# Optimization experiments

Hardware: AMD Instinct MI355X
Metric: run time of the kernel (lower is better)

Reference implementation:

```python
import jax, jax.numpy as jnp
import numpy as np
from jax import lax

DIM = 256
NH = 16          # num_heads; head_dim = DIM//NH == NH (required by scale broadcast)
HD = DIM // NH   # 16
HID = int(DIM * 1.0)  # mlp hidden (ffn_expansion_factor=1.0)
B, H, W = 4, 128, 128
EPS = 1e-5


def _conv(x, w, pad, groups=1):
    # x: NCHW, w: OIHW
    return lax.conv_general_dilated(x, w, (1, 1), [(pad, pad), (pad, pad)],
                                    dimension_numbers=('NCHW', 'OIHW', 'NCHW'),
                                    feature_group_count=groups)


def _ln(x, w, b):
    # WithBias LayerNorm over channel axis (torch does it in b,(hw),c layout -> axis=c)
    mu = x.mean(1, keepdims=True)
    var = ((x - mu) ** 2).mean(1, keepdims=True)
    return (x - mu) / jnp.sqrt(var + EPS) * w[None, :, None, None] + b[None, :, None, None]


def setup_inputs() -> dict:
    key = jax.random.key(0)
    ks = jax.random.split(key, 12)
    s = 0.02
    return {
        'x': jax.random.normal(ks[0], (B, DIM, H, W), jnp.float32),
        'ln1_w': jnp.ones((DIM,), jnp.float32),
        'ln1_b': jnp.zeros((DIM,), jnp.float32),
        'conv3_w': jax.random.normal(ks[1], (DIM, 1, 3, 3), jnp.float32) * s,
        'conv3_b': jnp.zeros((DIM,), jnp.float32),
        'conv5_w': jax.random.normal(ks[2], (DIM, 1, 5, 5), jnp.float32) * s,
        'conv5_b': jnp.zeros((DIM,), jnp.float32),
        'qkv_w': jax.random.normal(ks[3], (3 * DIM, DIM), jnp.float32) * s,  # 1x1 conv, no bias
        'scale': jnp.ones((NH, 1, 1), jnp.float32),
        'g1_w': jax.random.normal(ks[4], (DIM // 4, DIM), jnp.float32) * s,
        'g1_b': jnp.zeros((DIM // 4,), jnp.float32),
        'g2_w': jax.random.normal(ks[5], (2, DIM // 4), jnp.float32) * s,
        'g2_b': jnp.zeros((2,), jnp.float32),
        'proj_w': jax.random.normal(ks[6], (DIM, DIM), jnp.float32) * s,
        'proj_b': jnp.zeros((DIM,), jnp.float32),
        'ln2_w': jnp.ones((DIM,), jnp.float32),
        'ln2_b': jnp.zeros((DIM,), jnp.float32),
        'pin_w': jax.random.normal(ks[7], (2 * HID, DIM), jnp.float32) * s,  # 1x1, bias=False
        'dw_w': jax.random.normal(ks[8], (2 * HID, 2, 3, 3), jnp.float32) * s,  # groups=HID
        'pout_w': jax.random.normal(ks[9], (DIM, HID), jnp.float32) * s,
    }


def _forward(x, ln1_w, ln1_b, conv3_w, conv3_b, conv5_w, conv5_b, qkv_w, scale,
             g1_w, g1_b, g2_w, g2_b, proj_w, proj_b, ln2_w, ln2_b, pin_w, dw_w, pout_w):
    b, c, h, w = x.shape
    # ---- token mixer (CAFormer) ----
    y = _ln(x, ln1_w, ln1_b)
    conv_feat = (_conv(y, conv3_w, 1, groups=DIM) + conv3_b[None, :, None, None]
                 + _conv(y, conv5_w, 2, groups=DIM) + conv5_b[None, :, None, None])
    qkv = jnp.einsum('oc,bchw->bohw', qkv_w, y)  # (b, 3c, h, w)
    q, k, v = jnp.split(qkv.reshape(b, 3, NH, HD, h * w), 3, axis=1)
    q, k, v = q[:, 0], k[:, 0], v[:, 0]  # (b, nh, hd, h*w)
    # L2 normalize over entire flattened spatial extent (F.normalize, eps=1e-12)
    q = q / jnp.maximum(jnp.linalg.norm(q, axis=-1, keepdims=True), 1e-12)
    k = k / jnp.maximum(jnp.linalg.norm(k, axis=-1, keepdims=True), 1e-12)
    q4 = q.reshape(b, NH, HD, h, w)
    k4 = k.reshape(b, NH, HD, h, w)
    v4 = v.reshape(b, NH, HD, h, w)
    # scale (nh,1,1) right-aligned against (b,nh,hd,x,x): broadcasts along hd axis
    sc = scale.reshape(1, 1, NH, 1, 1)
    # horizontal (row) attention: per (b,head,hd-channel), rows attend to rows
    attn_h = jax.nn.softmax(jnp.einsum('bhdxy,bhdzy->bhdxz', q4, k4) * sc, axis=-1)
    out_h = jnp.einsum('bhdxz,bhdzy->bhdxy', attn_h, v4).reshape(b, c, h, w)
    # vertical (column) attention
    qt, kt, vt = (t.swapaxes(-1, -2) for t in (q4, k4, v4))  # (b,nh,hd,w,h)
    attn_v = jax.nn.softmax(jnp.einsum('bhdyx,bhdzx->bhdyz', qt, kt) * sc, axis=-1)
    out_v = jnp.einsum('bhdyz,bhdzx->bhdyx', attn_v, vt).swapaxes(-1, -2).reshape(b, c, h, w)
    attn_feat = out_h + out_v
    # gate: GAP -> 1x1 -> relu -> 1x1 -> softmax over the 2 branch logits
    gp = y.mean((2, 3))  # (b, c)
    g = jax.nn.relu(gp @ g1_w.T + g1_b)
    g = jax.nn.softmax(g @ g2_w.T + g2_b, axis=-1)  # (b, 2)
    cw = g[:, 0][:, None, None, None]
    aw = g[:, 1][:, None, None, None]
    mixed = cw * conv_feat + aw * attn_feat
    tm = jnp.einsum('oc,bchw->bohw', proj_w, mixed) + proj_b[None, :, None, None]
    x = x + tm
    # ---- MLP ----
    y2 = _ln(x, ln2_w, ln2_b)
    p = jnp.einsum('oc,bchw->bohw', pin_w, y2)  # (b, 2*HID, h, w)
    dwo = _conv(p, dw_w, 1, groups=HID)         # grouped 3x3, 2 ch per group
    x1, x2 = dwo[:, :HID], dwo[:, HID:]
    m = jax.nn.gelu(x1, approximate=False) * x2
    mlp = jnp.einsum('oc,bchw->bohw', pout_w, m)
    return x + mlp


def reference(x, ln1_w, ln1_b, conv3_w, conv3_b, conv5_w, conv5_b, qkv_w, scale,
              g1_w, g1_b, g2_w, g2_b, proj_w, proj_b, ln2_w, ln2_b, pin_w, dw_w, pout_w):
    return _forward(x, ln1_w, ln1_b, conv3_w, conv3_b, conv5_w, conv5_b, qkv_w, scale,
                    g1_w, g1_b, g2_w, g2_b, proj_w, proj_b, ln2_w, ln2_b, pin_w, dw_w, pout_w)
```

## Files before the change

kernel.cpp:

```cpp
#include <hip/hip_runtime.h>
#include <hip/hip_bf16.h>
#include <math.h>

#define DIMC 256
#define NB   4
#define HH   128
#define WW   128
#define HWs  16384
#define HID  256
#define C2   512
#define EPSf 1e-5f

typedef __hip_bfloat16 bf;
typedef unsigned short u16;
typedef unsigned int   u32;
typedef float f32x4  __attribute__((ext_vector_type(4)));
typedef u32   u32x4  __attribute__((ext_vector_type(4)));
typedef short bf16x8 __attribute__((ext_vector_type(8)));

__device__ __forceinline__ float b2f(bf v){ return __bfloat162float(v); }
__device__ __forceinline__ bf    f2b(float v){ return __float2bfloat16(v); }
__device__ __forceinline__ float ldf(const float* p){ return *p; }
__device__ __forceinline__ float ldf(const bf* p){ return __bfloat162float(*p); }
__device__ __forceinline__ void  sto(float* p, float v){ *p = v; }
__device__ __forceinline__ void  sto(bf* p, float v){ *p = f2b(v); }
__device__ __forceinline__ void unpack2(u32 u, float& a, float& b){
  union{u32 x; float f;} lo, hi;
  lo.x = u << 16; hi.x = u & 0xffff0000u;
  a = lo.f; b = hi.f;
}
__device__ __forceinline__ u32 pack2(float a, float b){
  bf h0 = f2b(a), h1 = f2b(b);
  return (u32)*(u16*)&h0 | ((u32)*(u16*)&h1 << 16);
}
__device__ __forceinline__ void unp4(uint2 u, float* d){
  unpack2(u.x, d[0], d[1]); unpack2(u.y, d[2], d[3]);
}

__device__ __forceinline__ float gelu_exact(float v){
  return 0.5f*v*(1.0f + erff(v*0.70710678118654752f));
}

__global__ __launch_bounds__(256) void cvt_kernel(const float* __restrict__ s,
    u16* __restrict__ d, int n){
  int i = blockIdx.x*256 + threadIdx.x;
  if (i < n){ bf h = f2b(s[i]); d[i] = *(u16*)&h; }
}

template<typename TI>
__global__ __launch_bounds__(256) void ln_kernel(const TI* __restrict__ x,
    const float* __restrict__ w, const float* __restrict__ bb, bf* __restrict__ y){
  int p = blockIdx.x*256 + threadIdx.x;
  int b  = p >> 14;
  int sp = p & (HWs-1);
  const TI* xb = x + (size_t)b*DIMC*HWs + sp;
  float s = 0.f, s2 = 0.f;
  for(int c=0;c<DIMC;c++){ float v = ldf(xb + (size_t)c*HWs); s += v; s2 += v*v; }
  float mu   = s * (1.0f/DIMC);
  float var  = s2 * (1.0f/DIMC) - mu*mu;
  float rinv = rsqrtf(var + EPSf);
  bf* yb = y + (size_t)b*DIMC*HWs + sp;
  for(int c=0;c<DIMC;c++){
    float v = ldf(xb + (size_t)c*HWs);
    yb[(size_t)c*HWs] = f2b((v - mu)*rinv*w[c] + bb[c]);
  }
}

__global__ __launch_bounds__(256) void gp_kernel(const bf* __restrict__ y, float* __restrict__ gp){
  int bc = blockIdx.x;
  const bf* pl = y + (size_t)bc*HWs;
  float s = 0.f;
  for(int i=threadIdx.x;i<HWs;i+=256) s += b2f(pl[i]);
  __shared__ float red[256];
  red[threadIdx.x] = s; __syncthreads();
  for(int o=128;o>0;o>>=1){
    if(threadIdx.x<o) red[threadIdx.x] += red[threadIdx.x+o];
    __syncthreads();
  }
  if(threadIdx.x==0) gp[bc] = red[0]*(1.0f/HWs);
}

__global__ __launch_bounds__(256) void gate_kernel(const float* __restrict__ gp,
    const float* __restrict__ g1w, const float* __restrict__ g1b,
    const float* __restrict__ g2w, const float* __restrict__ g2b,
    float* __restrict__ cwaw){
  __shared__ float h[NB][64];
  __shared__ float zz[NB][2];
  int t = threadIdx.x;
  int b = t >> 6, j = t & 63;
  const float* gpb = gp + b*DIMC;
  const float* wr  = g1w + j*DIMC;
  float s = g1b[j];
  for(int c=0;c<DIMC;c++) s += gpb[c]*wr[c];
  h[b][j] = fmaxf(s, 0.f);
  __syncthreads();
  if (t < 8){
    int b2 = t >> 1, o = t & 1;
    float z = g2b[o];
    const float* w2 = g2w + o*64;
    for(int q=0;q<64;q++) z += w2[q]*h[b2][q];
    zz[b2][o] = z;
  }
  __syncthreads();
  if (t < 4){
    float z0 = zz[t][0], z1 = zz[t][1];
    float mm = fmaxf(z0,z1);
    float e0 = __expf(z0-mm), e1 = __expf(z1-mm);
    float inv = 1.0f/(e0+e1);
    cwaw[2*t]   = e0*inv;
    cwaw[2*t+1] = e1*inv;
  }
}

__global__ __launch_bounds__(256) void dwconv_kernel(const bf* __restrict__ y,
    const float* __restrict__ w3, const float* __restrict__ b3,
    const float* __restrict__ w5, const float* __restrict__ b5,
    bf* __restrict__ out){
  int bi = blockIdx.x;
  int strip = bi & 7;
  int c  = (bi >> 3) & 255;
  int b  = bi >> 11;
  int t = threadIdx.x;
  int sx = t & 15, ry = t >> 4;
  int hy = strip*16 + ry;
  int x0 = sx << 3;
  const u16* pl = (const u16*)y + ((size_t)(b*DIMC + c))*HWs;

  float kc[25];
  #pragma unroll
  for(int i=0;i<25;i++) kc[i] = w5[c*25+i];
  #pragma unroll
  for(int di=0;di<3;di++)
    #pragma unroll
    for(int dj=0;dj<3;dj++)
      kc[(di+1)*5 + (dj+1)] += w3[c*9 + di*3 + dj];
  float bia = b3[c] + b5[c];

  float acc[8];
  #pragma unroll
  for(int j=0;j<8;j++) acc[j] = bia;

  #pragma unroll
  for(int di=-2; di<=2; di++){
    int yy = hy + di;
    float row[16];
    if ((unsigned)yy < 128u){
      const u16* rp = pl + yy*WW;
      uint2 z; z.x = 0u; z.y = 0u;
      uint2 c0 = (x0 > 0)   ? *(const uint2*)(rp + x0 - 4) : z;
      uint2 c1 = *(const uint2*)(rp + x0);
      uint2 c2 = *(const uint2*)(rp + x0 + 4);
      uint2 c3 = (x0 < 120) ? *(const uint2*)(rp + x0 + 8) : z;
      unp4(c0, row); unp4(c1, row+4); unp4(c2, row+8); unp4(c3, row+12);
    } else {
      #pragma unroll
      for(int j=0;j<16;j++) row[j] = 0.f;
    }
    #pragma unroll
    for(int dj=-2; dj<=2; dj++){
      float w = kc[(di+2)*5 + (dj+2)];
      #pragma unroll
      for(int j=0;j<8;j++) acc[j] += row[4+j+dj]*w;
    }
  }
  u32x4 res;
  #pragma unroll
  for(int q=0;q<4;q++) ((u32*)&res)[q] = pack2(acc[2*q], acc[2*q+1]);
  *(u32x4*)((u16*)out + ((size_t)(b*DIMC + c))*HWs + hy*WW + x0) = res;
}

__global__ __launch_bounds__(256) void dwconv2_glu_kernel(const bf* __restrict__ p,
    const float* __restrict__ w, bf* __restrict__ m){
  int bi = blockIdx.x;
  int strip = bi & 7;
  int op = (bi >> 3) & 127;
  int b  = bi >> 10;
  int o0 = op*2, o1 = o0+1;
  int t = threadIdx.x;
  int sx = t & 15, ry = t >> 4;
  int hy = strip*16 + ry;
  int x0 = sx << 3;
  const u16* p0 = (const u16*)p + ((size_t)b*C2 + o0)*HWs;
  const u16* p1 = p0 + HWs;
  const u16* p2 = p0 + (size_t)256*HWs;
  const u16* p3 = p2 + HWs;

  float KA0[9], KA1[9], KA2[9], KA3[9];
  float KB0[9], KB1[9], KB2[9], KB3[9];
  #pragma unroll
  for(int i=0;i<9;i++){
    KA0[i] = w[o0*18 + i];        KA1[i] = w[o0*18 + 9 + i];
    KA2[i] = w[(o0+256)*18 + i];  KA3[i] = w[(o0+256)*18 + 9 + i];
    KB0[i] = w[o1*18 + i];        KB1[i] = w[o1*18 + 9 + i];
    KB2[i] = w[(o1+256)*18 + i];  KB3[i] = w[(o1+256)*18 + 9 + i];
  }

  float a1A[8] = {}, a2A[8] = {}, a1B[8] = {}, a2B[8] = {};
  #pragma unroll
  for(int di=-1; di<=1; di++){
    int yy = hy + di;
    if ((unsigned)yy >= 128u) continue;
    int roff = yy*WW;
    float r0[16], r1[16], r2[16], r3[16];
    uint2 z; z.x = 0u; z.y = 0u;
    bool lo = (x0 > 0), hi = (x0 < 120);
    {
      const u16* rp = p0 + roff;
      uint2 c0 = lo ? *(const uint2*)(rp + x0 - 4) : z;
      uint2 c1 = *(const uint2*)(rp + x0);
      uint2 c2 = *(const uint2*)(rp + x0 + 4);
      uint2 c3 = hi ? *(const uint2*)(rp + x0 + 8) : z;
      unp4(c0, r0); unp4(c1, r0+4); unp4(c2, r0+8); unp4(c3, r0+12);
    }
    {
      const u16* rp = p1 + roff;
      uint2 c0 = lo ? *(const uint2*)(rp + x0 - 4) : z;
      uint2 c1 = *(const uint2*)(rp + x0);
      uint2 c2 = *(const uint2*)(rp + x0 + 4);
      uint2 c3 = hi ? *(const uint2*)(rp + x0 + 8) : z;
      unp4(c0, r1); unp4(c1, r1+4); unp4(c2, r1+8); unp4(c3, r1+12);
    }
    {
      const u16* rp = p2 + roff;
      uint2 c0 = lo ? *(const uint2*)(rp + x0 - 4) : z;
      uint2 c1 = *(const uint2*)(rp + x0);
      uint2 c2 = *(const uint2*)(rp + x0 + 4);
      uint2 c3 = hi ? *(const uint2*)(rp + x0 + 8) : z;
      unp4(c0, r2); unp4(c1, r2+4); unp4(c2, r2+8); unp4(c3, r2+12);
    }
    {
      const u16* rp = p3 + roff;
      uint2 c0 = lo ? *(const uint2*)(rp + x0 - 4) : z;
      uint2 c1 = *(const uint2*)(rp + x0);
      uint2 c2 = *(const uint2*)(rp + x0 + 4);
      uint2 c3 = hi ? *(const uint2*)(rp + x0 + 8) : z;
      unp4(c0, r3); unp4(c1, r3+4); unp4(c2, r3+8); unp4(c3, r3+12);
    }
    #pragma unroll
    for(int dj=-1; dj<=1; dj++){
      int ki = (di+1)*3 + (dj+1);
      #pragma unroll
      for(int j=0;j<8;j++){
        int ii = 4+j+dj;
        a1A[j] += r0[ii]*KA0[ki] + r1[ii]*KA1[ki];
        a2A[j] += r2[ii]*KA2[ki] + r3[ii]*KA3[ki];
        a1B[j] += r0[ii]*KB0[ki] + r1[ii]*KB1[ki];
        a2B[j] += r2[ii]*KB2[ki] + r3[ii]*KB3[ki];
      }
    }
  }
  size_t obase = ((size_t)(b*DIMC + o0))*HWs + hy*WW + x0;
  u32x4 resA, resB;
  #pragma unroll
  for(int q=0;q<4;q++){
    ((u32*)&resA)[q] = pack2(gelu_exact(a1A[2*q])*a2A[2*q],
                             gelu_exact(a1A[2*q+1])*a2A[2*q+1]);
    ((u32*)&resB)[q] = pack2(gelu_exact(a1B[2*q])*a2B[2*q],
                             gelu_exact(a1B[2*q+1])*a2B[2*q+1]);
  }
  *(u32x4*)((u16*)m + obase) = resA;
  *(u32x4*)((u16*)m + obase + HWs) = resB;
}

template<typename TRES, typename TOUT>
__global__ __launch_bounds__(256, 2) void mfma_gemm(
    const u16* __restrict__ Wb, const bf* __restrict__ act,
    const float* __restrict__ bias, const TRES* __restrict__ resid,
    TOUT* __restrict__ out, int Oc)
{
  __shared__ u16 As[2][4608];
  __shared__ u16 Bs[2][4096];
  int t  = threadIdx.x;
  int n0 = blockIdx.x * 128;
  int o0 = blockIdx.y * 128;
  int b  = n0 >> 14;
  int sp = n0 & (HWs-1);
  const u16* actu = (const u16*)act + (size_t)b*256*HWs + sp;

  int kp = t & 15;
  int ns = (t >> 4) << 3;
  int lane = t & 63;
  int wv = t >> 6;
  int wr = (wv >> 1) << 6;
  int wc = (wv & 1) << 6;
  int fr = lane & 15;
  int kg = lane >> 4;
  int arow = t >> 1;
  int ahalf = (t & 1) << 4;

  f32x4 acc[4][4] = {};

  auto loadB = [&](int ks, u32x4& u, u32x4& v){
    const u16* r0 = actu + (size_t)(ks*32 + 2*kp)*HWs + ns;
    u = *(const u32x4*)r0;
    v = *(const u32x4*)(r0 + HWs);
  };
  auto writeB = [&](const u32x4& u, const u32x4& v, int buf){
    u32 w0=(u.x&0xffffu)|(v.x<<16), w1=(u.x>>16)|(v.x&0xffff0000u);
    u32 w2=(u.y&0xffffu)|(v.y<<16), w3=(u.y>>16)|(v.y&0xffff0000u);
    u32 w4=(u.z&0xffffu)|(v.z<<16), w5=(u.z>>16)|(v.z&0xffff0000u);
    u32 w6=(u.w&0xffffu)|(v.w<<16), w7=(u.w>>16)|(v.w&0xffff0000u);
    u16* bp = Bs[buf];
    int c0 = kp*2;
    *(u32*)&bp[(ns+0)*32+c0]=w0; *(u32*)&bp[(ns+1)*32+c0]=w1;
    *(u32*)&bp[(ns+2)*32+c0]=w2; *(u32*)&bp[(ns+3)*32+c0]=w3;
    *(u32*)&bp[(ns+4)*32+c0]=w4; *(u32*)&bp[(ns+5)*32+c0]=w5;
    *(u32*)&bp[(ns+6)*32+c0]=w6; *(u32*)&bp[(ns+7)*32+c0]=w7;
  };
  auto loadA = [&](int ks, u32x4& a0, u32x4& a1){
    const u16* ap = Wb + (size_t)(o0+arow)*256 + ks*32 + ahalf;
    a0 = *(const u32x4*)ap;
    a1 = *(const u32x4*)(ap + 8);
  };
  auto writeA = [&](const u32x4& a0, const u32x4& a1, int buf){
    u16* dst = &As[buf][arow*36 + ahalf];
    *(u32x4*)dst = a0;
    *(u32x4*)(dst+8) = a1;
  };

  {
    u32x4 bu, bvv, a0, a1;
    loadB(0, bu, bvv); loadA(0, a0, a1);
    writeB(bu, bvv, 0); writeA(a0, a1, 0);
  }
  #pragma unroll
  for(int ks=0; ks<8; ++ks){
    int cur = ks & 1;
    __syncthreads();
    u32x4 bu, bvv, a0, a1;
    if (ks < 7){ loadB(ks+1, bu, bvv); loadA(ks+1, a0, a1); }
    bf16x8 af[4], bfr[4];
    #pragma unroll
    for(int j=0;j<4;j++)
      bfr[j] = *(const bf16x8*)&Bs[cur][(wc + j*16 + fr)*32 + kg*8];
    #pragma unroll
    for(int i=0;i<4;i++)
      af[i] = *(const bf16x8*)&As[cur][(wr + i*16 + fr)*36 + kg*8];
    #pragma unroll
    for(int i=0;i<4;i++)
      #pragma unroll
      for(int j=0;j<4;j++)
        acc[i][j] = __builtin_amdgcn_mfma_f32_16x16x32_bf16(af[i], bfr[j], acc[i][j], 0, 0, 0);
    if (ks < 7){ writeB(bu, bvv, cur^1); writeA(a0, a1, cur^1); }
  }

  #pragma unroll
  for(int i=0;i<4;i++){
    #pragma unroll
    for(int reg=0;reg<4;reg++){
      int o = o0 + wr + i*16 + kg*4 + reg;
      size_t rowoff = ((size_t)b*Oc + o)*HWs + sp + wc + fr;
      float bia = bias ? bias[o] : 0.f;
      #pragma unroll
      for(int j=0;j<4;j++){
        float val = acc[i][j][reg] + bia;
        size_t pidx = rowoff + (size_t)(j*16);
        if (resid) val += ldf(resid + pidx);
        sto(out + pidx, val);
      }
    }
  }
}

#define SWB(r,c2) ((r)*256 + ((c2) ^ (((r)&7)<<4)))

__global__ __launch_bounds__(256, 2) void attn_mfma(const bf* __restrict__ qkv,
    const float* __restrict__ scale, bf* __restrict__ outp,
    const bf* __restrict__ conv, const float* __restrict__ cwaw){
  __shared__ u16 LB0[16384];
  __shared__ u16 LB1[16384];
  __shared__ float2 red2[4];
  int s  = blockIdx.x;
  int b  = s >> 8;
  int ch = s & 255;
  const u16* qp = (const u16*)qkv + ((size_t)b*768 + ch)*HWs;
  const u16* kp = qp + (size_t)256*HWs;
  const u16* vp = qp + (size_t)512*HWs;
  int t = threadIdx.x;

  int lane = t & 63, wvi = t >> 6;
  int fr = lane & 15, kg = lane >> 4;
  int nb = wvi << 5;
  int rr = t >> 1, hb = (t & 1) << 7;

  auto stage_nat = [&](const u16* src, u16* dst){
    #pragma unroll
    for(int i=0;i<8;i++){
      int c2 = hb + i*16;
      u32x4 v = *(const u32x4*)((const char*)src + rr*256 + c2);
      *(u32x4*)((char*)dst + SWB(rr, c2)) = v;
    }
  };
  auto stage_nat_sum = [&](const u16* src, u16* dst) -> float {
    float ssum = 0.f;
    #pragma unroll
    for(int i=0;i<8;i++){
      int c2 = hb + i*16;
      u32x4 v = *(const u32x4*)((const char*)src + rr*256 + c2);
      *(u32x4*)((char*)dst + SWB(rr, c2)) = v;
      #pragma unroll
      for(int q=0;q<4;q++){
        float a0, a1;
        unpack2(((u32*)&v)[q], a0, a1);
        ssum += a0*a0 + a1*a1;
      }
    }
    return ssum;
  };
  auto stage_tr = [&](const u16* src, u16* dst){
    int kp2 = (t & 15)*2, cs = (t >> 4) << 3;
    #pragma unroll
    for(int base=0;base<128;base+=32){
      int sr = base + kp2;
      u32x4 u = *(const u32x4*)(src + sr*128 + cs);
      u32x4 v = *(const u32x4*)(src + (sr+1)*128 + cs);
      #pragma unroll
      for(int j=0;j<8;j++){
        u32 uw = ((const u32*)&u)[j>>1];
        u32 vw = ((const u32*)&v)[j>>1];
        u32 wv = (j&1) ? ((uw>>16) | (vw & 0xffff0000u))
                       : ((uw & 0xffffu) | (vw<<16));
        *(u32*)((char*)dst + SWB(cs+j, sr*2)) = wv;
      }
    }
  };

  f32x4 acc[8][2];
  f32x4 oacc[8][2];
  const f32x4 vzero = {};
  float ls = 0.f;

  auto mmloop = [&](const u16* afsrc, const u16* bfsrc, f32x4 (&A)[8][2]){
    #pragma unroll
    for(int kk=0;kk<128;kk+=32){
      int kb2 = kk*2 + kg*16;
      bf16x8 b0 = *(const bf16x8*)((const char*)bfsrc + SWB(nb+fr,    kb2));
      bf16x8 b1 = *(const bf16x8*)((const char*)bfsrc + SWB(nb+16+fr, kb2));
      #pragma unroll
      for(int mt=0;mt<8;mt++){
        bf16x8 a0 = *(const bf16x8*)((const char*)afsrc + SWB(mt*16+fr, kb2));
        A[mt][0] = __builtin_amdgcn_mfma_f32_16x16x32_bf16(a0, b0, A[mt][0], 0, 0, 0);
        A[mt][1] = __builtin_amdgcn_mfma_f32_16x16x32_bf16(a0, b1, A[mt][1], 0, 0, 0);
      }
    }
  };

  auto writeCT = [&](u16* dst, f32x4 (&A)[8][2]){
    #pragma unroll
    for(int nt=0;nt<2;nt++){
      int n = nb + nt*16 + fr;
      #pragma unroll
      for(int mt=0;mt<8;mt++){
        #pragma unroll
        for(int pr=0;pr<2;pr++){
          u32 wv = pack2(A[mt][nt][pr*2], A[mt][nt][pr*2+1]);
          int z2 = (mt*16 + kg*4 + pr*2)*2;
          *(u32*)((char*)dst + SWB(n, z2)) = wv;
        }
      }
    }
  };

  auto softmax = [&](){
    #pragma unroll
    for(int nt=0;nt<2;nt++){
      float mx = -1e30f;
      #pragma unroll
      for(int mt=0;mt<8;mt++)
        #pragma unroll
        for(int rg=0;rg<4;rg++){
          acc[mt][nt][rg] *= ls;
          mx = fmaxf(mx, acc[mt][nt][rg]);
        }
      mx = fmaxf(mx, __shfl_xor(mx,16));
      mx = fmaxf(mx, __shfl_xor(mx,32));
      float sm = 0.f;
      #pragma unroll
      for(int mt=0;mt<8;mt++)
        #pragma unroll
        for(int rg=0;rg<4;rg++){
          float e = __expf(acc[mt][nt][rg]-mx);
          acc[mt][nt][rg] = e; sm += e;
        }
      sm += __shfl_xor(sm,16);
      sm += __shfl_xor(sm,32);
      float inv = 1.0f/sm;
      #pragma unroll
      for(int mt=0;mt<8;mt++)
        #pragma unroll
        for(int rg=0;rg<4;rg++)
          acc[mt][nt][rg] *= inv;
    }
  };

  float sk = stage_nat_sum(kp, LB0);
  float sq = stage_nat_sum(qp, LB1);
  #pragma unroll
  for(int off=1; off<64; off<<=1){
    sq += __shfl_xor(sq, off);
    sk += __shfl_xor(sk, off);
  }
  if (lane == 0) red2[wvi] = make_float2(sq, sk);
  __syncthreads();
  {
    float tq = 0.f, tk = 0.f;
    #pragma unroll
    for(int wI=0;wI<4;wI++){ tq += red2[wI].x; tk += red2[wI].y; }
    float nq = fmaxf(sqrtf(tq), 1e-12f);
    float nk = fmaxf(sqrtf(tk), 1e-12f);
    ls = scale[ch & 15] / (nq*nk);
  }
  #pragma unroll
  for(int mt=0;mt<8;mt++){ acc[mt][0]=vzero; acc[mt][1]=vzero; }
  mmloop(LB0, LB1, acc);
  softmax();
  __syncthreads();
  writeCT(LB0, acc);
  stage_tr(vp, LB1);
  __syncthreads();
  #pragma unroll
  for(int mt=0;mt<8;mt++){ oacc[mt][0]=vzero; oacc[mt][1]=vzero; }
  mmloop(LB1, LB0, oacc);
  __syncthreads();

  stage_tr(kp, LB0); stage_tr(qp, LB1);
  __syncthreads();
  #pragma unroll
  for(int mt=0;mt<8;mt++){ acc[mt][0]=vzero; acc[mt][1]=vzero; }
  mmloop(LB0, LB1, acc);
  softmax();
  __syncthreads();
  writeCT(LB0, acc);
  stage_nat(vp, LB1);
  __syncthreads();
  mmloop(LB0, LB1, oacc);
  __syncthreads();

  writeCT(LB0, oacc);
  __syncthreads();

  float cw = cwaw[2*b], aw = cwaw[2*b+1];
  const u16* cp = (const u16*)conv + ((size_t)b*DIMC + ch)*HWs;
  bf* op = outp + ((size_t)b*DIMC + ch)*HWs;
  #pragma unroll
  for(int i=0;i<8;i++){
    int c2 = hb + i*16;
    u32x4 ov = *(const u32x4*)((char*)LB0 + SWB(rr, c2));
    u32x4 cv = *(const u32x4*)(cp + rr*128 + c2/2);
    u32x4 res;
    #pragma unroll
    for(int q=0;q<4;q++){
      float o0,o1,c0,c1;
      unpack2(((u32*)&ov)[q], o0, o1);
      unpack2(((u32*)&cv)[q], c0, c1);
      ((u32*)&res)[q] = pack2(cw*c0 + aw*o0, cw*c1 + aw*o1);
    }
    *(u32x4*)((u16*)op + rr*128 + c2/2) = res;
  }
}

extern "C" void kernel_launch(void* const* d_in, const int* in_sizes, int n_in,
                              void* d_out, int out_size, void* d_ws, size_t ws_size,
                              hipStream_t stream){
  (void)in_sizes; (void)n_in; (void)out_size; (void)ws_size;
  const float* x       = (const float*)d_in[0];
  const float* ln1_w   = (const float*)d_in[1];
  const float* ln1_b   = (const float*)d_in[2];
  const float* conv3_w = (const float*)d_in[3];
  const float* conv3_b = (const float*)d_in[4];
  const float* conv5_w = (const float*)d_in[5];
  const float* conv5_b = (const float*)d_in[6];
  const float* qkv_w   = (const float*)d_in[7];
  const float* scale   = (const float*)d_in[8];
  const float* g1_w    = (const float*)d_in[9];
  const float* g1_b    = (const float*)d_in[10];
  const float* g2_w    = (const float*)d_in[11];
  const float* g2_b    = (const float*)d_in[12];
  const float* proj_w  = (const float*)d_in[13];
  const float* proj_b  = (const float*)d_in[14];
  const float* ln2_w   = (const float*)d_in[15];
  const float* ln2_b   = (const float*)d_in[16];
  const float* pin_w   = (const float*)d_in[17];
  const float* dw_w    = (const float*)d_in[18];
  const float* pout_w  = (const float*)d_in[19];
  float* out = (float*)d_out;
  char* wsb  = (char*)d_ws;

  const size_t MB = 1024*1024;
  bf* y    = (bf*)(wsb +   0*MB);
  bf* conv = (bf*)(wsb +  32*MB);
  bf* qkv  = (bf*)(wsb +  64*MB);
  bf* attnf= (bf*)(wsb +   0*MB);
  bf* xnew = (bf*)(wsb +  64*MB);
  bf* y2   = (bf*)(wsb +  96*MB);
  bf* p    = (bf*)(wsb +   0*MB);
  bf* m    = (bf*)(wsb +  96*MB);
  u16* Wqkv  = (u16*)(wsb + 160*MB);
  u16* Wproj = Wqkv + 196608;
  u16* Wpin  = Wproj + 65536;
  u16* Wpout = Wpin + 131072;
  float* gp     = (float*)(Wpout + 65536);
  float* cwaw   = gp + 1024;

  cvt_kernel<<<768,256,0,stream>>>(qkv_w,  Wqkv, 196608);
  cvt_kernel<<<256,256,0,stream>>>(proj_w, Wproj, 65536);
  cvt_kernel<<<512,256,0,stream>>>(pin_w,  Wpin, 131072);
  cvt_kernel<<<256,256,0,stream>>>(pout_w, Wpout, 65536);

  ln_kernel<float><<<256,256,0,stream>>>(x, ln1_w, ln1_b, y);
  gp_kernel<<<1024,256,0,stream>>>(y, gp);
  gate_kernel<<<1,256,0,stream>>>(gp, g1_w, g1_b, g2_w, g2_b, cwaw);
  dwconv_kernel<<<8192,256,0,stream>>>(y, conv3_w, conv3_b, conv5_w, conv5_b, conv);
  mfma_gemm<float,bf><<<dim3(512,6),256,0,stream>>>(Wqkv, y, nullptr,
                                        (const float*)nullptr, qkv, 768);
  attn_mfma<<<1024,256,0,stream>>>(qkv, scale, attnf, conv, cwaw);
  mfma_gemm<float,bf><<<dim3(512,2),256,0,stream>>>(Wproj, attnf, proj_b, x, xnew, 256);
  ln_kernel<bf><<<256,256,0,stream>>>(xnew, ln2_w, ln2_b, y2);
  mfma_gemm<float,bf><<<dim3(512,4),256,0,stream>>>(Wpin, y2, nullptr,
                                        (const float*)nullptr, p, 512);
  dwconv2_glu_kernel<<<4096,256,0,stream>>>(p, dw_w, m);
  mfma_gemm<bf,float><<<dim3(512,2),256,0,stream>>>(Wpout, m, nullptr, xnew, out, 256);
}
```

Measured before the change: 430.0 us.

## Fuse LN2 into pin GEMM, prefetch attention operands into registers, extend LDS swizzle

The second LayerNorm is split in two: a stats kernel computes per-pixel mean and rstd, and the pin GEMM normalizes its activation tiles while staging them into LDS. This removes the write and reread of the normalized y2 tensor. The attention kernel now loads the next Q/K/V tiles and the conv features into registers before the preceding matmul phase, overlapping global loads with compute. The LDS swizzle gains an extra XOR bit to reduce bank conflicts. The cost is higher register pressure and redundant normalization arithmetic across the four output tiles of the GEMM.

```diff
diff --git a/kernel.cpp b/kernel.cpp
--- a/kernel.cpp
+++ b/kernel.cpp
@@ -66,6 +66,20 @@
   }
 }
 
+__global__ __launch_bounds__(256) void stats_kernel(const bf* __restrict__ x,
+    float* __restrict__ st){
+  int p = blockIdx.x*256 + threadIdx.x;
+  int b  = p >> 14;
+  int sp = p & (HWs-1);
+  const bf* xb = x + (size_t)b*DIMC*HWs + sp;
+  float s = 0.f, s2 = 0.f;
+  for(int c=0;c<DIMC;c++){ float v = b2f(xb[(size_t)c*HWs]); s += v; s2 += v*v; }
+  float mu   = s * (1.0f/DIMC);
+  float var  = s2 * (1.0f/DIMC) - mu*mu;
+  st[2*p]   = mu;
+  st[2*p+1] = rsqrtf(var + EPSf);
+}
+
 __global__ __launch_bounds__(256) void gp_kernel(const bf* __restrict__ y, float* __restrict__ gp){
   int bc = blockIdx.x;
   const bf* pl = y + (size_t)bc*HWs;
@@ -262,11 +276,13 @@
   *(u32x4*)((u16*)m + obase + HWs) = resB;
 }
 
-template<typename TRES, typename TOUT>
+template<int MODE, typename TRES, typename TOUT>
 __global__ __launch_bounds__(256, 2) void mfma_gemm(
     const u16* __restrict__ Wb, const bf* __restrict__ act,
     const float* __restrict__ bias, const TRES* __restrict__ resid,
-    TOUT* __restrict__ out, int Oc)
+    TOUT* __restrict__ out, int Oc,
+    const float* __restrict__ stats, const float* __restrict__ lnw,
+    const float* __restrict__ lnb)
 {
   __shared__ u16 As[2][4608];
   __shared__ u16 Bs[2][4096];
@@ -290,16 +306,45 @@
 
   f32x4 acc[4][4] = {};
 
+  float sbuf[16];
+  if (MODE==1){
+    const float* sb = stats + 2*((size_t)b*HWs + sp + ns);
+    *(f32x4*)&sbuf[0]  = *(const f32x4*)sb;
+    *(f32x4*)&sbuf[4]  = *(const f32x4*)(sb+4);
+    *(f32x4*)&sbuf[8]  = *(const f32x4*)(sb+8);
+    *(f32x4*)&sbuf[12] = *(const f32x4*)(sb+12);
+  }
+
   auto loadB = [&](int ks, u32x4& u, u32x4& v){
     const u16* r0 = actu + (size_t)(ks*32 + 2*kp)*HWs + ns;
     u = *(const u32x4*)r0;
     v = *(const u32x4*)(r0 + HWs);
   };
-  auto writeB = [&](const u32x4& u, const u32x4& v, int buf){
-    u32 w0=(u.x&0xffffu)|(v.x<<16), w1=(u.x>>16)|(v.x&0xffff0000u);
-    u32 w2=(u.y&0xffffu)|(v.y<<16), w3=(u.y>>16)|(v.y&0xffff0000u);
-    u32 w4=(u.z&0xffffu)|(v.z<<16), w5=(u.z>>16)|(v.z&0xffff0000u);
-    u32 w6=(u.w&0xffffu)|(v.w<<16), w7=(u.w>>16)|(v.w&0xffff0000u);
+  auto writeB = [&](const u32x4& u, const u32x4& v, int buf, int ks){
+    u32 w0,w1,w2,w3,w4,w5,w6,w7;
+    if (MODE==0){
+      w0=(u.x&0xffffu)|(v.x<<16); w1=(u.x>>16)|(v.x&0xffff0000u);
+      w2=(u.y&0xffffu)|(v.y<<16); w3=(u.y>>16)|(v.y&0xffff0000u);
+      w4=(u.z&0xffffu)|(v.z<<16); w5=(u.z>>16)|(v.z&0xffff0000u);
+      w6=(u.w&0xffffu)|(v.w<<16); w7=(u.w>>16)|(v.w&0xffff0000u);
+    } else {
+      float A[8], B[8];
+      unpack2(u.x,A[0],A[1]); unpack2(u.y,A[2],A[3]);
+      unpack2(u.z,A[4],A[5]); unpack2(u.w,A[6],A[7]);
+      unpack2(v.x,B[0],B[1]); unpack2(v.y,B[2],B[3]);
+      unpack2(v.z,B[4],B[5]); unpack2(v.w,B[6],B[7]);
+      int k0 = ks*32 + 2*kp;
+      float wa = lnw[k0], ba = lnb[k0], wb2 = lnw[k0+1], bb2 = lnb[k0+1];
+      u32 wt[8];
+      #pragma unroll
+      for(int j=0;j<8;j++){
+        float na = (A[j]-sbuf[2*j])*sbuf[2*j+1]*wa + ba;
+        float nb2 = (B[j]-sbuf[2*j])*sbuf[2*j+1]*wb2 + bb2;
+        wt[j] = pack2(na, nb2);
+      }
+      w0=wt[0]; w1=wt[1]; w2=wt[2]; w3=wt[3];
+      w4=wt[4]; w5=wt[5]; w6=wt[6]; w7=wt[7];
+    }
     u16* bp = Bs[buf];
     int c0 = kp*2;
     *(u32*)&bp[(ns+0)*32+c0]=w0; *(u32*)&bp[(ns+1)*32+c0]=w1;
@@ -321,7 +366,7 @@
   {
     u32x4 bu, bvv, a0, a1;
     loadB(0, bu, bvv); loadA(0, a0, a1);
-    writeB(bu, bvv, 0); writeA(a0, a1, 0);
+    writeB(bu, bvv, 0, 0); writeA(a0, a1, 0);
   }
   #pragma unroll
   for(int ks=0; ks<8; ++ks){
@@ -341,7 +386,7 @@
       #pragma unroll
       for(int j=0;j<4;j++)
         acc[i][j] = __builtin_amdgcn_mfma_f32_16x16x32_bf16(af[i], bfr[j], acc[i][j], 0, 0, 0);
-    if (ks < 7){ writeB(bu, bvv, cur^1); writeA(a0, a1, cur^1); }
+    if (ks < 7){ writeB(bu, bvv, cur^1, ks+1); writeA(a0, a1, cur^1); }
   }
 
   #pragma unroll
@@ -362,7 +407,7 @@
   }
 }
 
-#define SWB(r,c2) ((r)*256 + ((c2) ^ (((r)&7)<<4)))
+#define SWB(r,c2) ((r)*256 + ((c2) ^ ((((r)&7)<<4)) ^ ((((r)>>3)&1)<<6)))
 
 __global__ __launch_bounds__(256, 2) void attn_mfma(const bf* __restrict__ qkv,
     const float* __restrict__ scale, bf* __restrict__ outp,
@@ -382,42 +427,48 @@
   int fr = lane & 15, kg = lane >> 4;
   int nb = wvi << 5;
   int rr = t >> 1, hb = (t & 1) << 7;
-
-  auto stage_nat = [&](const u16* src, u16* dst){
+  int kp2 = (t & 15)*2, cs = (t >> 4) << 3;
+
+  auto nat_load = [&](const u16* src, u32x4* R){
+    #pragma unroll
+    for(int i=0;i<8;i++)
+      R[i] = *(const u32x4*)((const char*)src + rr*256 + hb + i*16);
+  };
+  auto nat_write = [&](const u32x4* R, u16* dst){
+    #pragma unroll
+    for(int i=0;i<8;i++)
+      *(u32x4*)((char*)dst + SWB(rr, hb + i*16)) = R[i];
+  };
+  auto nat_write_sum = [&](const u32x4* R, u16* dst) -> float {
+    float ssum = 0.f;
     #pragma unroll
     for(int i=0;i<8;i++){
-      int c2 = hb + i*16;
-      u32x4 v = *(const u32x4*)((const char*)src + rr*256 + c2);
-      *(u32x4*)((char*)dst + SWB(rr, c2)) = v;
-    }
-  };
-  auto stage_nat_sum = [&](const u16* src, u16* dst) -> float {
-    float ssum = 0.f;
-    #pragma unroll
-    for(int i=0;i<8;i++){
-      int c2 = hb + i*16;
-      u32x4 v = *(const u32x4*)((const char*)src + rr*256 + c2);
-      *(u32x4*)((char*)dst + SWB(rr, c2)) = v;
+      *(u32x4*)((char*)dst + SWB(rr, hb + i*16)) = R[i];
       #pragma unroll
       for(int q=0;q<4;q++){
         float a0, a1;
-        unpack2(((u32*)&v)[q], a0, a1);
+        unpack2(((const u32*)&R[i])[q], a0, a1);
         ssum += a0*a0 + a1*a1;
       }
     }
     return ssum;
   };
-  auto stage_tr = [&](const u16* src, u16* dst){
-    int kp2 = (t & 15)*2, cs = (t >> 4) << 3;
-    #pragma unroll
-    for(int base=0;base<128;base+=32){
-      int sr = base + kp2;
-      u32x4 u = *(const u32x4*)(src + sr*128 + cs);
-      u32x4 v = *(const u32x4*)(src + (sr+1)*128 + cs);
+  auto tr_load = [&](const u16* src, u32x4* R){
+    #pragma unroll
+    for(int bi=0;bi<4;bi++){
+      int sr = bi*32 + kp2;
+      R[2*bi]   = *(const u32x4*)(src + sr*128 + cs);
+      R[2*bi+1] = *(const u32x4*)(src + (sr+1)*128 + cs);
+    }
+  };
+  auto tr_write = [&](const u32x4* R, u16* dst){
+    #pragma unroll
+    for(int bi=0;bi<4;bi++){
+      int sr = bi*32 + kp2;
       #pragma unroll
       for(int j=0;j<8;j++){
-        u32 uw = ((const u32*)&u)[j>>1];
-        u32 vw = ((const u32*)&v)[j>>1];
+        u32 uw = ((const u32*)&R[2*bi])[j>>1];
+        u32 vw = ((const u32*)&R[2*bi+1])[j>>1];
         u32 wv = (j&1) ? ((uw>>16) | (vw & 0xffff0000u))
                        : ((uw & 0xffffu) | (vw<<16));
         *(u32*)((char*)dst + SWB(cs+j, sr*2)) = wv;
@@ -493,8 +544,13 @@
     }
   };
 
-  float sk = stage_nat_sum(kp, LB0);
-  float sq = stage_nat_sum(qp, LB1);
+  u32x4 RK[8], RQ[8], RV[8];
+
+  nat_load(kp, RK);
+  nat_load(qp, RQ);
+  tr_load(vp, RV);
+  float sk = nat_write_sum(RK, LB0);
+  float sq = nat_write_sum(RQ, LB1);
   #pragma unroll
   for(int off=1; off<64; off<<=1){
     sq += __shfl_xor(sq, off);
@@ -510,29 +566,44 @@
     float nk = fmaxf(sqrtf(tk), 1e-12f);
     ls = scale[ch & 15] / (nq*nk);
   }
+
   #pragma unroll
   for(int mt=0;mt<8;mt++){ acc[mt][0]=vzero; acc[mt][1]=vzero; }
   mmloop(LB0, LB1, acc);
   softmax();
   __syncthreads();
+
   writeCT(LB0, acc);
-  stage_tr(vp, LB1);
-  __syncthreads();
+  tr_write(RV, LB1);
+  tr_load(kp, RK);
+  tr_load(qp, RQ);
+  __syncthreads();
+
   #pragma unroll
   for(int mt=0;mt<8;mt++){ oacc[mt][0]=vzero; oacc[mt][1]=vzero; }
   mmloop(LB1, LB0, oacc);
   __syncthreads();
 
-  stage_tr(kp, LB0); stage_tr(qp, LB1);
-  __syncthreads();
+  tr_write(RK, LB0);
+  tr_write(RQ, LB1);
+  nat_load(vp, RV);
+  __syncthreads();
+
   #pragma unroll
   for(int mt=0;mt<8;mt++){ acc[mt][0]=vzero; acc[mt][1]=vzero; }
   mmloop(LB0, LB1, acc);
   softmax();
   __syncthreads();
+
   writeCT(LB0, acc);
-  stage_nat(vp, LB1);
-  __syncthreads();
+  nat_write(RV, LB1);
+  const u16* cp = (const u16*)conv + ((size_t)b*DIMC + ch)*HWs;
+  u32x4 RC[8];
+  #pragma unroll
+  for(int i=0;i<8;i++)
+    RC[i] = *(const u32x4*)(cp + rr*128 + (hb>>1) + i*8);
+  __syncthreads();
+
   mmloop(LB0, LB1, oacc);
   __syncthreads();
 
@@ -540,22 +611,20 @@
   __syncthreads();
 
   float cw = cwaw[2*b], aw = cwaw[2*b+1];
-  const u16* cp = (const u16*)conv + ((size_t)b*DIMC + ch)*HWs;
   bf* op = outp + ((size_t)b*DIMC + ch)*HWs;
   #pragma unroll
   for(int i=0;i<8;i++){
     int c2 = hb + i*16;
     u32x4 ov = *(const u32x4*)((char*)LB0 + SWB(rr, c2));
-    u32x4 cv = *(const u32x4*)(cp + rr*128 + c2/2);
     u32x4 res;
     #pragma unroll
     for(int q=0;q<4;q++){
       float o0,o1,c0,c1;
       unpack2(((u32*)&ov)[q], o0, o1);
-      unpack2(((u32*)&cv)[q], c0, c1);
+      unpack2(((const u32*)&RC[i])[q], c0, c1);
       ((u32*)&res)[q] = pack2(cw*c0 + aw*o0, cw*c1 + aw*o1);
     }
-    *(u32x4*)((u16*)op + rr*128 + c2/2) = res;
+    *(u32x4*)((u16*)op + rr*128 + (hb>>1) + i*8) = res;
   }
 }
 
@@ -592,7 +661,7 @@
   bf* qkv  = (bf*)(wsb +  64*MB);
   bf* attnf= (bf*)(wsb +   0*MB);
   bf* xnew = (bf*)(wsb +  64*MB);
-  bf* y2   = (bf*)(wsb +  96*MB);
+  float* stats = (float*)(wsb + 96*MB);
   bf* p    = (bf*)(wsb +   0*MB);
   bf* m    = (bf*)(wsb +  96*MB);
   u16* Wqkv  = (u16*)(wsb + 160*MB);
@@ -611,13 +680,15 @@
   gp_kernel<<<1024,256,0,stream>>>(y, gp);
   gate_kernel<<<1,256,0,stream>>>(gp, g1_w, g1_b, g2_w, g2_b, cwaw);
   dwconv_kernel<<<8192,256,0,stream>>>(y, conv3_w, conv3_b, conv5_w, conv5_b, conv);
-  mfma_gemm<float,bf><<<dim3(512,6),256,0,stream>>>(Wqkv, y, nullptr,
-                                        (const float*)nullptr, qkv, 768);
+  mfma_gemm<0,float,bf><<<dim3(512,6),256,0,stream>>>(Wqkv, y, nullptr,
+      (const float*)nullptr, qkv, 768, nullptr, nullptr, nullptr);
   attn_mfma<<<1024,256,0,stream>>>(qkv, scale, attnf, conv, cwaw);
-  mfma_gemm<float,bf><<<dim3(512,2),256,0,stream>>>(Wproj, attnf, proj_b, x, xnew, 256);
-  ln_kernel<bf><<<256,256,0,stream>>>(xnew, ln2_w, ln2_b, y2);
-  mfma_gemm<float,bf><<<dim3(512,4),256,0,stream>>>(Wpin, y2, nullptr,
-                                        (const float*)nullptr, p, 512);
+  mfma_gemm<0,float,bf><<<dim3(512,2),256,0,stream>>>(Wproj, attnf, proj_b, x,
+      xnew, 256, nullptr, nullptr, nullptr);
+  stats_kernel<<<256,256,0,stream>>>(xnew, stats);
+  mfma_gemm<1,float,bf><<<dim3(512,4),256,0,stream>>>(Wpin, xnew, nullptr,
+      (const float*)nullptr, p, 512, stats, ln2_w, ln2_b);
   dwconv2_glu_kernel<<<4096,256,0,stream>>>(p, dw_w, m);
-  mfma_gemm<bf,float><<<dim3(512,2),256,0,stream>>>(Wpout, m, nullptr, xnew, out, 256);
-}
+  mfma_gemm<0,bf,float><<<dim3(512,2),256,0,stream>>>(Wpout, m, nullptr, xnew,
+      out, 256, nullptr, nullptr, nullptr);
+}
```

New measurement: 439.7 us. 2.3% more time.

## Prefetch QKV and conv tiles into registers and reuse LDS for transposes

Applied to the files above, without the earlier changes.

The attention kernel now loads K, Q and the transposed V tile into registers up front. The transposed K/Q copies are built from the already staged LDS tiles instead of being reloaded from global memory. The second V load and the conv feature load are issued early so their global latency overlaps the MFMA and softmax work. The LDS swizzle also gains an extra XOR bit to cut bank conflicts. The cost is much higher register pressure from the 32 u32x4 prefetch buffers under launch_bounds(256,2), which could cause spills.

```diff
diff --git a/kernel.cpp b/kernel.cpp
--- a/kernel.cpp
+++ b/kernel.cpp
@@ -362,7 +362,7 @@
   }
 }
 
-#define SWB(r,c2) ((r)*256 + ((c2) ^ (((r)&7)<<4)))
+#define SWB(r,c2) ((r)*256 + ((c2) ^ ((((r)&7)<<4)) ^ ((((r)>>3)&1)<<6)))
 
 __global__ __launch_bounds__(256, 2) void attn_mfma(const bf* __restrict__ qkv,
     const float* __restrict__ scale, bf* __restrict__ outp,
@@ -382,42 +382,56 @@
   int fr = lane & 15, kg = lane >> 4;
   int nb = wvi << 5;
   int rr = t >> 1, hb = (t & 1) << 7;
-
-  auto stage_nat = [&](const u16* src, u16* dst){
+  int kp2 = (t & 15)*2, cs = (t >> 4) << 3;
+
+  auto nat_load = [&](const u16* src, u32x4* R){
+    #pragma unroll
+    for(int i=0;i<8;i++)
+      R[i] = *(const u32x4*)((const char*)src + rr*256 + hb + i*16);
+  };
+  auto nat_write = [&](const u32x4* R, u16* dst){
+    #pragma unroll
+    for(int i=0;i<8;i++)
+      *(u32x4*)((char*)dst + SWB(rr, hb + i*16)) = R[i];
+  };
+  auto nat_write_sum = [&](const u32x4* R, u16* dst) -> float {
+    float ssum = 0.f;
     #pragma unroll
     for(int i=0;i<8;i++){
-      int c2 = hb + i*16;
-      u32x4 v = *(const u32x4*)((const char*)src + rr*256 + c2);
-      *(u32x4*)((char*)dst + SWB(rr, c2)) = v;
-    }
-  };
-  auto stage_nat_sum = [&](const u16* src, u16* dst) -> float {
-    float ssum = 0.f;
-    #pragma unroll
-    for(int i=0;i<8;i++){
-      int c2 = hb + i*16;
-      u32x4 v = *(const u32x4*)((const char*)src + rr*256 + c2);
-      *(u32x4*)((char*)dst + SWB(rr, c2)) = v;
+      *(u32x4*)((char*)dst + SWB(rr, hb + i*16)) = R[i];
       #pragma unroll
       for(int q=0;q<4;q++){
         float a0, a1;
-        unpack2(((u32*)&v)[q], a0, a1);
+        unpack2(((const u32*)&R[i])[q], a0, a1);
         ssum += a0*a0 + a1*a1;
       }
     }
     return ssum;
   };
-  auto stage_tr = [&](const u16* src, u16* dst){
-    int kp2 = (t & 15)*2, cs = (t >> 4) << 3;
-    #pragma unroll
-    for(int base=0;base<128;base+=32){
-      int sr = base + kp2;
-      u32x4 u = *(const u32x4*)(src + sr*128 + cs);
-      u32x4 v = *(const u32x4*)(src + (sr+1)*128 + cs);
+  auto tr_load = [&](const u16* src, u32x4* R){
+    #pragma unroll
+    for(int bi=0;bi<4;bi++){
+      int sr = bi*32 + kp2;
+      R[2*bi]   = *(const u32x4*)(src + sr*128 + cs);
+      R[2*bi+1] = *(const u32x4*)(src + (sr+1)*128 + cs);
+    }
+  };
+  auto tr_load_lds = [&](const u16* lb, u32x4* R){
+    #pragma unroll
+    for(int bi=0;bi<4;bi++){
+      int sr = bi*32 + kp2;
+      R[2*bi]   = *(const u32x4*)((const char*)lb + SWB(sr,   cs*2));
+      R[2*bi+1] = *(const u32x4*)((const char*)lb + SWB(sr+1, cs*2));
+    }
+  };
+  auto tr_write = [&](const u32x4* R, u16* dst){
+    #pragma unroll
+    for(int bi=0;bi<4;bi++){
+      int sr = bi*32 + kp2;
       #pragma unroll
       for(int j=0;j<8;j++){
-        u32 uw = ((const u32*)&u)[j>>1];
-        u32 vw = ((const u32*)&v)[j>>1];
+        u32 uw = ((const u32*)&R[2*bi])[j>>1];
+        u32 vw = ((const u32*)&R[2*bi+1])[j>>1];
         u32 wv = (j&1) ? ((uw>>16) | (vw & 0xffff0000u))
                        : ((uw & 0xffffu) | (vw<<16));
         *(u32*)((char*)dst + SWB(cs+j, sr*2)) = wv;
@@ -493,8 +507,13 @@
     }
   };
 
-  float sk = stage_nat_sum(kp, LB0);
-  float sq = stage_nat_sum(qp, LB1);
+  u32x4 RK[8], RQ[8], RV[8];
+
+  nat_load(kp, RK);
+  nat_load(qp, RQ);
+  tr_load(vp, RV);
+  float sk = nat_write_sum(RK, LB0);
+  float sq = nat_write_sum(RQ, LB1);
   #pragma unroll
   for(int off=1; off<64; off<<=1){
     sq += __shfl_xor(sq, off);
@@ -510,29 +529,44 @@
     float nk = fmaxf(sqrtf(tk), 1e-12f);
     ls = scale[ch & 15] / (nq*nk);
   }
+
   #pragma unroll
   for(int mt=0;mt<8;mt++){ acc[mt][0]=vzero; acc[mt][1]=vzero; }
   mmloop(LB0, LB1, acc);
   softmax();
-  __syncthreads();
+  tr_load_lds(LB0, RK);
+  tr_load_lds(LB1, RQ);
+  __syncthreads();
+
   writeCT(LB0, acc);
-  stage_tr(vp, LB1);
-  __syncthreads();
+  tr_write(RV, LB1);
+  __syncthreads();
+
   #pragma unroll
   for(int mt=0;mt<8;mt++){ oacc[mt][0]=vzero; oacc[mt][1]=vzero; }
   mmloop(LB1, LB0, oacc);
   __syncthreads();
 
-  stage_tr(kp, LB0); stage_tr(qp, LB1);
-  __syncthreads();
+  tr_write(RK, LB0);
+  tr_write(RQ, LB1);
+  nat_load(vp, RV);
+  __syncthreads();
+
   #pragma unroll
   for(int mt=0;mt<8;mt++){ acc[mt][0]=vzero; acc[mt][1]=vzero; }
   mmloop(LB0, LB1, acc);
   softmax();
   __syncthreads();
+
   writeCT(LB0, acc);
-  stage_nat(vp, LB1);
-  __syncthreads();
+  nat_write(RV, LB1);
+  const u16* cp = (const u16*)conv + ((size_t)b*DIMC + ch)*HWs;
+  u32x4 RC[8];
+  #pragma unroll
+  for(int i=0;i<8;i++)
+    RC[i] = *(const u32x4*)(cp + rr*128 + (hb>>1) + i*8);
+  __syncthreads();
+
   mmloop(LB0, LB1, oacc);
   __syncthreads();
 
@@ -540,22 +574,20 @@
   __syncthreads();
 
   float cw = cwaw[2*b], aw = cwaw[2*b+1];
-  const u16* cp = (const u16*)conv + ((size_t)b*DIMC + ch)*HWs;
   bf* op = outp + ((size_t)b*DIMC + ch)*HWs;
   #pragma unroll
   for(int i=0;i<8;i++){
     int c2 = hb + i*16;
     u32x4 ov = *(const u32x4*)((char*)LB0 + SWB(rr, c2));
-    u32x4 cv = *(const u32x4*)(cp + rr*128 + c2/2);
     u32x4 res;
     #pragma unroll
     for(int q=0;q<4;q++){
       float o0,o1,c0,c1;
       unpack2(((u32*)&ov)[q], o0, o1);
-      unpack2(((u32*)&cv)[q], c0, c1);
+      unpack2(((const u32*)&RC[i])[q], c0, c1);
       ((u32*)&res)[q] = pack2(cw*c0 + aw*o0, cw*c1 + aw*o1);
     }
-    *(u32x4*)((u16*)op + rr*128 + c2/2) = res;
+    *(u32x4*)((u16*)op + rr*128 + (hb>>1) + i*8) = res;
   }
 }
 
```

Measured after the change: 419.6 us. 1.02x faster.
